# Kernel optimization log

Hardware: AMD Instinct MI355X
Metric: run time of the kernel (lower is better)

## Reference

```python
import jax, jax.numpy as jnp
import numpy as np

LN_EPS = 1e-5


def setup_inputs() -> dict:
    key = jax.random.key(0)
    ks = jax.random.split(key, 10)
    B, T, S, C = 8, 1024, 2048, 1024
    sd = 1.0 / np.sqrt(C)
    return {
        "x": jax.random.normal(ks[0], (B, T, C), jnp.float32),
        "lfb_feats": jax.random.normal(ks[1], (B, S, C), jnp.float32),
        "theta_w": jax.random.normal(ks[2], (C, C), jnp.float32) * sd,
        "theta_b": jax.random.normal(ks[3], (C,), jnp.float32) * 0.01,
        "phi_w": jax.random.normal(ks[4], (C, C), jnp.float32) * sd,
        "phi_b": jax.random.normal(ks[5], (C,), jnp.float32) * 0.01,
        "gi_w": jax.random.normal(ks[6], (C, C), jnp.float32) * sd,
        "gi_b": jax.random.normal(ks[7], (C,), jnp.float32) * 0.01,
        "ln_g": jnp.ones((C,), jnp.float32),
        "ln_b": jnp.zeros((C,), jnp.float32),
        "fc_w": jax.random.normal(ks[8], (C, C), jnp.float32) * sd,
        "fc_b": jax.random.normal(ks[9], (C,), jnp.float32) * 0.01,
    }


def _layernorm(h, g, b):
    mu = jnp.mean(h, axis=-1, keepdims=True)
    var = jnp.var(h, axis=-1, keepdims=True)
    return (h - mu) * jax.lax.rsqrt(var + LN_EPS) * g + b


def reference(x, lfb_feats, theta_w, theta_b, phi_w, phi_b, gi_w, gi_b,
              ln_g, ln_b, fc_w, fc_b):
    # x: [B,T,C], lfb_feats: [B,S,C]. 1x1 Conv1d == per-token linear on channels.
    C = x.shape[-1]
    scale = jnp.sqrt(jnp.asarray(C, x.dtype))  # NOTE: 1/sqrt(1/C) = sqrt(C) (as in source)
    theta = jnp.einsum('btc,oc->bto', x, theta_w) + theta_b          # [B,T,C]
    phi = jnp.einsum('bsc,oc->bso', lfb_feats, phi_w) + phi_b        # [B,S,C]
    gi = jnp.einsum('bsc,oc->bso', lfb_feats, gi_w) + gi_b           # [B,S,C]
    attn = jax.nn.softmax(jnp.einsum('btc,bsc->bts', theta, phi) * scale, axis=-1)
    out = jnp.einsum('bts,bsc->btc', attn, gi)                       # [B,T,C]
    out = jax.nn.relu(_layernorm(out, ln_g, ln_b))
    out = jnp.einsum('btc,oc->bto', out, fc_w) + fc_b                # fc (dropout = identity at eval)
    return out + x                                                   # residual, [B,T,C]
```

## Files before the change

kernel.cpp:

```cpp
#include <hip/hip_runtime.h>


#define BM 128
#define BN 128
#define BK 64

typedef __attribute__((ext_vector_type(8))) short short8;
typedef __attribute__((ext_vector_type(4))) float f32x4;
typedef __attribute__((ext_vector_type(4))) unsigned short us4;

enum { MODE_SPLIT = 0, MODE_TRANS = 1, MODE_F32 = 2, MODE_FINAL = 3 };

__device__ __forceinline__ float b2f(unsigned short u) {
  union { unsigned int i; float f; } x;
  x.i = ((unsigned int)u) << 16;
  return x.f;
}
__device__ __forceinline__ unsigned short f2b(float f) {
  unsigned int u = __float_as_uint(f);
  unsigned int r = (u + 0x7FFFu + ((u >> 16) & 1u)) >> 16;
  return (unsigned short)r;
}

__device__ __forceinline__ void async_cp16(const unsigned short* g,
                                           unsigned short* l) {
  __builtin_amdgcn_global_load_lds(
      (const __attribute__((address_space(1))) void*)g,
      (__attribute__((address_space(3))) void*)l, 16, 0, 0);
}

__global__ __launch_bounds__(256) void split_xlfb(
    const float* __restrict__ lfb, const float* __restrict__ x,
    const float* __restrict__ g, unsigned short* __restrict__ ls,
    unsigned short* __restrict__ xs, float* __restrict__ v, int Ms) {
  const int id = blockIdx.x;
  const int t = threadIdx.x;
  const int c = t * 4;
  if (id < Ms) {
    __shared__ float red[4];
    f32x4 xv = *(const f32x4*)&lfb[(size_t)id * 1024 + c];
    f32x4 gg = *(const f32x4*)&g[c];
    us4 hi, lo;
    float s = 0.f;
#pragma unroll
    for (int i = 0; i < 4; ++i) {
      hi[i] = f2b(xv[i]);
      lo[i] = f2b(xv[i] - b2f(hi[i]));
      s += xv[i] * gg[i];
    }
    *(us4*)&ls[(size_t)id * 2048 + c] = hi;
    *(us4*)&ls[(size_t)id * 2048 + 1024 + c] = lo;
    for (int o = 32; o; o >>= 1) s += __shfl_xor(s, o, 64);
    if ((t & 63) == 0) red[t >> 6] = s;
    __syncthreads();
    if (t == 0) v[id] = red[0] + red[1] + red[2] + red[3];
  } else {
    const int r = id - Ms;
    f32x4 xv = *(const f32x4*)&x[(size_t)r * 1024 + c];
    us4 hi, lo;
#pragma unroll
    for (int i = 0; i < 4; ++i) {
      hi[i] = f2b(xv[i]);
      lo[i] = f2b(xv[i] - b2f(hi[i]));
    }
    *(us4*)&xs[(size_t)r * 2048 + c] = hi;
    *(us4*)&xs[(size_t)r * 2048 + 1024 + c] = lo;
  }
}

__global__ __launch_bounds__(256) void cvt2_bf16(const float* __restrict__ s0,
                                                 unsigned short* __restrict__ d0,
                                                 const float* __restrict__ s1,
                                                 unsigned short* __restrict__ d1) {
  int b = blockIdx.x;
  const float* src = (b < 1024) ? s0 : s1;
  unsigned short* dst = (b < 1024) ? d0 : d1;
  int g = (b & 1023) * 256 + threadIdx.x;
  f32x4 v = *(const f32x4*)&src[g * 4];
  us4 o;
#pragma unroll
  for (int i = 0; i < 4; ++i) o[i] = f2b(v[i]);
  *(us4*)&dst[(size_t)g * 4] = o;
}

__global__ __launch_bounds__(256) void transpose_split2(
    const float* __restrict__ W0, unsigned short* __restrict__ T0,
    const float* __restrict__ W1, unsigned short* __restrict__ T1) {
  __shared__ float tile[64][65];
  const int sel = blockIdx.y >> 4;
  const float* W = sel ? W1 : W0;
  unsigned short* T = sel ? T1 : T0;
  const int bo = (blockIdx.y & 15) * 64;
  const int bc = blockIdx.x * 64;
  const int t = threadIdx.x;
  const int tr = t >> 4;
  const int tc = (t & 15) * 4;
#pragma unroll
  for (int i = 0; i < 4; ++i) {
    f32x4 v = *(const f32x4*)&W[(size_t)(bo + tr + 16 * i) * 1024 + bc + tc];
#pragma unroll
    for (int j = 0; j < 4; ++j) tile[tr + 16 * i][tc + j] = v[j];
  }
  __syncthreads();
#pragma unroll
  for (int i = 0; i < 4; ++i) {
    const int c = bc + tr + 16 * i;
    us4 hi, lo;
#pragma unroll
    for (int j = 0; j < 4; ++j) {
      float v = tile[tc + j][tr + 16 * i];
      hi[j] = f2b(v);
      lo[j] = f2b(v - b2f(hi[j]));
    }
    *(us4*)&T[(size_t)c * 2048 + bo + tc] = hi;
    *(us4*)&T[(size_t)c * 2048 + 1024 + bo + tc] = lo;
  }
}

__global__ __launch_bounds__(256) void make_g(
    const unsigned short* __restrict__ tB, const float* __restrict__ bth,
    float* __restrict__ g) {
  const int d = blockIdx.x * 4 + (threadIdx.x >> 6);
  const int lane = threadIdx.x & 63;
  float s = 0.f;
#pragma unroll
  for (int i = 0; i < 4; ++i) {
    const int o0 = lane * 4 + i * 256;
    us4 h = *(const us4*)&tB[(size_t)d * 2048 + o0];
    us4 lo = *(const us4*)&tB[(size_t)d * 2048 + 1024 + o0];
    f32x4 bb = *(const f32x4*)&bth[o0];
#pragma unroll
    for (int j = 0; j < 4; ++j) s += (b2f(h[j]) + b2f(lo[j])) * bb[j];
  }
  for (int o = 32; o; o >>= 1) s += __shfl_xor(s, o, 64);
  if (lane == 0) g[d] = s;
}

__global__ __launch_bounds__(256) void reduce_g(const float* __restrict__ P,
                                                unsigned short* __restrict__ Gs) {
  const int d = blockIdx.x;
  const int c = threadIdx.x * 4;
  f32x4 s = *(const f32x4*)&P[(size_t)d * 1024 + c];
#pragma unroll
  for (int z = 1; z < 8; ++z) {
    f32x4 p = *(const f32x4*)&P[(size_t)z * 1048576 + (size_t)d * 1024 + c];
#pragma unroll
    for (int i = 0; i < 4; ++i) s[i] += p[i];
  }
  us4 hi, lo;
#pragma unroll
  for (int i = 0; i < 4; ++i) {
    hi[i] = f2b(s[i]);
    lo[i] = f2b(s[i] - b2f(hi[i]));
  }
  *(us4*)&Gs[(size_t)d * 2048 + c] = hi;
  *(us4*)&Gs[(size_t)d * 2048 + 1024 + c] = lo;
}

template <int MODE>
__global__ __launch_bounds__(256, 4) void gemm_bt(
    const unsigned short* __restrict__ A, const unsigned short* __restrict__ B,
    void* __restrict__ Cout, const float* __restrict__ bias,
    const float* __restrict__ resid, int M, int N, int K, int lda, int ldb,
    int ldc, long long sA, long long sB, long long sC, long long sBias,
    int awrap, int awoff, int bwrap, int bwoff, int NBk, int MBk, int mbx,
    int swz, int kzoff) {
  __shared__ __align__(16) unsigned short As[BM * BK];
  __shared__ __align__(16) unsigned short Bs[BN * BK];

  const int tid = threadIdx.x;
  const int l = tid & 63;
  const int w = tid >> 6;
  const int wm = w >> 1, wn = w & 1;
  const int ln = l & 15, lq = l >> 4;

  int bmi, bni, bzi;
  {
    const int id = blockIdx.x;
    if (swz == 1) {
      bzi = id & 7;
      const int r = id >> 3;
      bmi = r % mbx;
      bni = r / mbx;
    } else if (swz == 2) {
      bzi = 0;
      const int r = id >> 3;
      bmi = (id & 7) * mbx + r % mbx;
      bni = r / mbx;
    } else {
      bni = id % NBk;
      const int rem = id / NBk;
      bmi = rem % MBk;
      bzi = rem / MBk;
    }
  }
  const int bm = bmi * BM;
  const int bn = bni * BN;
  const unsigned short* Ab = A + (size_t)bzi * (size_t)sA;
  const unsigned short* Bb = B + (size_t)bzi * (size_t)sB;
  const float* bz = bias ? bias + (size_t)bzi * (size_t)sBias : nullptr;
  const int kbase = bzi * kzoff;

  const int arow = tid >> 3;
  const int acol = (((tid & 7) ^ ((tid >> 3) & 7)) * 8);
  const int ldsbase = (tid & 0xC0) * 8;

  f32x4 acc[4][4];
#pragma unroll
  for (int i = 0; i < 4; ++i)
#pragma unroll
    for (int j = 0; j < 4; ++j) acc[i][j] = (f32x4){0.f, 0.f, 0.f, 0.f};

  const int sw = ln & 7;

  for (int k0 = 0; k0 < K; k0 += BK) {
    const int kg = k0 + kbase;
    const int ka = (kg < awrap) ? kg : kg - awoff;
    const int kb = (kg < bwrap) ? kg : kg - bwoff;
#pragma unroll
    for (int it = 0; it < 4; ++it) {
      const int r = it * 32 + arow;
      async_cp16(Ab + (size_t)(bm + r) * lda + ka + acol,
                 &As[it * 2048 + ldsbase]);
    }
#pragma unroll
    for (int it = 0; it < 4; ++it) {
      const int r = it * 32 + arow;
      async_cp16(Bb + (size_t)(bn + r) * ldb + kb + acol,
                 &Bs[it * 2048 + ldsbase]);
    }
    __syncthreads();

#pragma unroll
    for (int ks = 0; ks < 2; ++ks) {
      short8 a[4], b[4];
      const int kof = ((ks * 4 + lq) ^ sw) * 8;
#pragma unroll
      for (int i = 0; i < 4; ++i)
        a[i] = *(const short8*)&As[(wm * 64 + i * 16 + ln) * BK + kof];
#pragma unroll
      for (int j = 0; j < 4; ++j)
        b[j] = *(const short8*)&Bs[(wn * 64 + j * 16 + ln) * BK + kof];
#pragma unroll
      for (int i = 0; i < 4; ++i)
#pragma unroll
        for (int j = 0; j < 4; ++j)
          acc[i][j] = __builtin_amdgcn_mfma_f32_16x16x32_bf16(a[i], b[j],
                                                              acc[i][j], 0, 0, 0);
    }
    __syncthreads();
  }

  float* Cf = (float*)Cout + (size_t)bzi * (size_t)sC;
  unsigned short* Cb = (unsigned short*)Cout + (size_t)bzi * (size_t)sC;

  if constexpr (MODE == MODE_TRANS) {
#pragma unroll
    for (int i = 0; i < 4; ++i) {
      const int gm0 = bm + wm * 64 + i * 16 + lq * 4;
      const int bt = gm0 >> 11;
      const int sr = gm0 & 2047;
#pragma unroll
      for (int j = 0; j < 4; ++j) {
        const int gn = bn + wn * 64 + j * 16 + ln;
        const float bv2 = (bz != nullptr) ? bz[gn] : 0.f;
        us4 o;
#pragma unroll
        for (int r = 0; r < 4; ++r) o[r] = f2b(acc[i][j][r] + bv2);
        *(us4*)&Cb[(size_t)bt * 2097152 + (size_t)gn * 2048 + sr] = o;
      }
    }
  } else {
#pragma unroll
    for (int j = 0; j < 4; ++j) {
      const int gn = bn + wn * 64 + j * 16 + ln;
      const float bv2 = (bz != nullptr) ? bz[gn] : 0.f;
#pragma unroll
      for (int i = 0; i < 4; ++i) {
        const int gm0 = bm + wm * 64 + i * 16 + lq * 4;
#pragma unroll
        for (int r = 0; r < 4; ++r) {
          const int gm = gm0 + r;
          const float v = acc[i][j][r] + bv2;
          if constexpr (MODE == MODE_SPLIT) {
            unsigned short hi = f2b(v);
            Cb[(size_t)gm * ldc + gn] = hi;
            Cb[(size_t)gm * ldc + gn + (ldc >> 1)] = f2b(v - b2f(hi));
          } else if constexpr (MODE == MODE_F32) {
            Cf[(size_t)gm * ldc + gn] = v;
          } else if constexpr (MODE == MODE_FINAL) {
            const size_t idx = (size_t)gm * ldc + gn;
            Cf[idx] = v + resid[idx];
          }
        }
      }
    }
  }
}

__device__ __forceinline__ void ld8f(const unsigned short* Lb, int roff, int ln,
                                     int lq, int sw, short8* a) {
#pragma unroll
  for (int mi = 0; mi < 4; ++mi)
#pragma unroll
    for (int ks = 0; ks < 2; ++ks)
      a[mi * 2 + ks] = *(const short8*)&Lb[(roff + mi * 16 + ln) * 64 +
                                           (((ks * 4 + lq) ^ sw) * 8)];
}
__device__ __forceinline__ void ld4f(const unsigned short* Lb, int roff, int ln,
                                     int lq, int sw, short8* b) {
#pragma unroll
  for (int ni = 0; ni < 2; ++ni)
#pragma unroll
    for (int ks = 0; ks < 2; ++ks)
      b[ni * 2 + ks] = *(const short8*)&Lb[(roff + ni * 16 + ln) * 64 +
                                           (((ks * 4 + lq) ^ sw) * 8)];
}
template <int MH, int NH>
__device__ __forceinline__ void mfmaQ(f32x4 (&acc)[8][4], const short8* a,
                                      const short8* b) {
  __builtin_amdgcn_s_setprio(1);
#pragma unroll
  for (int mi = 0; mi < 4; ++mi)
#pragma unroll
    for (int ni = 0; ni < 2; ++ni)
#pragma unroll
      for (int ks = 0; ks < 2; ++ks)
        acc[MH * 4 + mi][NH * 2 + ni] = __builtin_amdgcn_mfma_f32_16x16x32_bf16(
            a[mi * 2 + ks], b[ni * 2 + ks], acc[MH * 4 + mi][NH * 2 + ni], 0, 0,
            0);
  __builtin_amdgcn_s_setprio(0);
}

template <int MODE>
__global__ __launch_bounds__(512, 1) void gemm8(
    const unsigned short* __restrict__ A, const unsigned short* __restrict__ B,
    void* __restrict__ Cout, const float* __restrict__ bias, int M, int N,
    int K, int lda, int ldb, int ldc, long long sA, long long sB, long long sC,
    long long sBias, int awrap, int awoff, int bwrap, int bwoff, int NBk,
    int MBk, int mbx, int swz) {
  __shared__ __align__(16) unsigned short lds[2][4][8192];

  const int tid = threadIdx.x;
  const int l = tid & 63;
  const int w = tid >> 6;
  const int wm = w >> 2;
  const int wn = w & 3;
  const int ln = l & 15, lq = l >> 4;
  const int sw = ln & 7;

  int bmi, bni, bzi;
  {
    const int id = blockIdx.x;
    if (swz == 1) {
      bzi = id & 7;
      const int r = id >> 3;
      bmi = r % mbx;
      bni = r / mbx;
    } else if (swz == 2) {
      bzi = 0;
      const int r = id >> 3;
      bmi = (id & 7) * mbx + r % mbx;
      bni = r / mbx;
    } else {
      bni = id % NBk;
      const int rem = id / NBk;
      bmi = rem % MBk;
      bzi = rem / MBk;
    }
  }
  const int bm = bmi * 256;
  const int bn = bni * 256;
  const unsigned short* Ab = A + (size_t)bzi * (size_t)sA;
  const unsigned short* Bb = B + (size_t)bzi * (size_t)sB;
  const float* bz = bias ? bias + (size_t)bzi * (size_t)sBias : nullptr;

  const int srow = tid >> 3;
  const int schk = ((tid & 7) ^ ((tid >> 3) & 7)) * 8;
  const int sdst0 = (tid & 448) * 8;

  auto stageA = [&](int d, int half, int kk) {
#pragma unroll
    for (int j = 0; j < 2; ++j)
      async_cp16(Ab + (size_t)(bm + half * 128 + srow + j * 64) * lda + kk +
                     schk,
                 &lds[d][half][sdst0 + j * 4096]);
  };
  auto stageB = [&](int d, int half, int kk) {
#pragma unroll
    for (int j = 0; j < 2; ++j)
      async_cp16(Bb + (size_t)(bn + half * 128 + srow + j * 64) * ldb + kk +
                     schk,
                 &lds[d][2 + half][sdst0 + j * 4096]);
  };
  auto wrapA = [&](int kg) { return (kg < awrap) ? kg : kg - awoff; };
  auto wrapB = [&](int kg) { return (kg < bwrap) ? kg : kg - bwoff; };

  f32x4 acc[8][4];
#pragma unroll
  for (int i = 0; i < 8; ++i)
#pragma unroll
    for (int j = 0; j < 4; ++j) acc[i][j] = (f32x4){0.f, 0.f, 0.f, 0.f};

  const int nt = K >> 6;

  stageA(0, 0, wrapA(0));
  stageA(0, 1, wrapA(0));
  stageB(0, 0, wrapB(0));
  stageB(0, 1, wrapB(0));
  if (nt > 1) {
    stageB(1, 0, wrapB(64));
    stageB(1, 1, wrapB(64));
    asm volatile("s_waitcnt vmcnt(4)" : : : "memory");
  } else {
    asm volatile("s_waitcnt vmcnt(0)" : : : "memory");
  }
  __builtin_amdgcn_s_barrier();

  const unsigned short* LA;
  const unsigned short* LB;
  short8 a0[8], a1[8], b0[4], b1[4];
  const int broff = (wn & 1) * 64;
  const int bslot = 2 + (wn >> 1);

  for (int t = 0; t < nt; ++t) {
    const int d = t & 1;
    LA = &lds[d][wm][0];
    LB = &lds[d][bslot][0];
    ld8f(LA, 0, ln, lq, sw, a0);
    ld4f(LB, broff, ln, lq, sw, b0);
    if (t + 1 < nt) stageA(d ^ 1, 0, wrapA((t + 1) * 64));
    __builtin_amdgcn_s_barrier();
    asm volatile("s_waitcnt lgkmcnt(0)" : : : "memory");
    __builtin_amdgcn_sched_barrier(0);
    mfmaQ<0, 0>(acc, a0, b0);
    __builtin_amdgcn_s_barrier();
    ld4f(LB, broff + 32, ln, lq, sw, b1);
    if (t + 1 < nt) stageA(d ^ 1, 1, wrapA((t + 1) * 64));
    __builtin_amdgcn_s_barrier();
    asm volatile("s_waitcnt lgkmcnt(0)" : : : "memory");
    __builtin_amdgcn_sched_barrier(0);
    mfmaQ<0, 1>(acc, a0, b1);
    __builtin_amdgcn_s_barrier();
    ld8f(LA, 64, ln, lq, sw, a1);
    if (t + 2 < nt) stageB(d, 0, wrapB((t + 2) * 64));
    __builtin_amdgcn_s_barrier();
    asm volatile("s_waitcnt lgkmcnt(0)" : : : "memory");
    __builtin_amdgcn_sched_barrier(0);
    mfmaQ<1, 1>(acc, a1, b1);
    __builtin_amdgcn_s_barrier();
    if (t + 2 < nt) stageB(d, 1, wrapB((t + 2) * 64));
    __builtin_amdgcn_s_barrier();
    mfmaQ<1, 0>(acc, a1, b0);
    if (t + 2 < nt) {
      asm volatile("s_waitcnt vmcnt(4)" : : : "memory");
    } else {
      asm volatile("s_waitcnt vmcnt(0)" : : : "memory");
    }
    __builtin_amdgcn_s_barrier();
  }

  float* Cf = (float*)Cout + (size_t)bzi * (size_t)sC;
  unsigned short* Cb = (unsigned short*)Cout;

  if constexpr (MODE == MODE_TRANS) {
#pragma unroll
    for (int mi = 0; mi < 8; ++mi) {
      const int gm0 = bm + wm * 128 + mi * 16 + lq * 4;
      const int bt = gm0 >> 11;
      const int sr = gm0 & 2047;
#pragma unroll
      for (int ni = 0; ni < 4; ++ni) {
        const int gn = bn + wn * 64 + ni * 16 + ln;
        const float bv2 = (bz != nullptr) ? bz[gn] : 0.f;
        us4 o;
#pragma unroll
        for (int r = 0; r < 4; ++r) o[r] = f2b(acc[mi][ni][r] + bv2);
        *(us4*)&Cb[(size_t)bt * 2097152 + (size_t)gn * 2048 + sr] = o;
      }
    }
  } else {
#pragma unroll
    for (int ni = 0; ni < 4; ++ni) {
      const int gn = bn + wn * 64 + ni * 16 + ln;
      const float bv2 = (bz != nullptr) ? bz[gn] : 0.f;
#pragma unroll
      for (int mi = 0; mi < 8; ++mi) {
        const int gm0 = bm + wm * 128 + mi * 16 + lq * 4;
#pragma unroll
        for (int r = 0; r < 4; ++r)
          Cf[(size_t)(gm0 + r) * ldc + gn] = acc[mi][ni][r] + bv2;
      }
    }
  }
}

__global__ __launch_bounds__(256) void softmax_rows(
    const float* __restrict__ logit, unsigned short* __restrict__ attn) {
  const int row = blockIdx.x;
  const float* L = logit + (size_t)row * 2048;
  unsigned short* O = attn + (size_t)row * 2048;
  const int t = threadIdx.x;
  __shared__ float red[8];

  f32x4 v0 = *(const f32x4*)&L[t * 4];
  f32x4 v1 = *(const f32x4*)&L[t * 4 + 1024];
  float m = fmaxf(fmaxf(fmaxf(v0[0], v0[1]), fmaxf(v0[2], v0[3])),
                  fmaxf(fmaxf(v1[0], v1[1]), fmaxf(v1[2], v1[3])));
  for (int o = 32; o; o >>= 1) m = fmaxf(m, __shfl_xor(m, o, 64));
  if ((t & 63) == 0) red[t >> 6] = m;
  __syncthreads();
  m = fmaxf(fmaxf(red[0], red[1]), fmaxf(red[2], red[3]));

  float e[8];
  float s = 0.f;
#pragma unroll
  for (int i = 0; i < 4; ++i) { e[i] = __expf(32.f * (v0[i] - m)); s += e[i]; }
#pragma unroll
  for (int i = 0; i < 4; ++i) { e[4 + i] = __expf(32.f * (v1[i] - m)); s += e[4 + i]; }
  for (int o = 32; o; o >>= 1) s += __shfl_xor(s, o, 64);
  if ((t & 63) == 0) red[4 + (t >> 6)] = s;
  __syncthreads();
  s = red[4] + red[5] + red[6] + red[7];
  const float inv = 1.f / s;
  us4 o0, o1;
#pragma unroll
  for (int i = 0; i < 4; ++i) { o0[i] = f2b(e[i] * inv); o1[i] = f2b(e[4 + i] * inv); }
  *(us4*)&O[t * 4] = o0;
  *(us4*)&O[t * 4 + 1024] = o1;
}

__global__ __launch_bounds__(256) void ln_relu(
    const float* __restrict__ X, const float* __restrict__ g,
    const float* __restrict__ b, unsigned short* __restrict__ H) {
  const int row = blockIdx.x;
  const float* x = X + (size_t)row * 1024;
  unsigned short* h = H + (size_t)row * 1024;
  const int t = threadIdx.x;
  __shared__ float red[8];
  f32x4 v = *(const f32x4*)&x[t * 4];
  float s = v[0] + v[1] + v[2] + v[3];
  float q = v[0] * v[0] + v[1] * v[1] + v[2] * v[2] + v[3] * v[3];
  for (int o = 32; o; o >>= 1) {
    s += __shfl_xor(s, o, 64);
    q += __shfl_xor(q, o, 64);
  }
  if ((t & 63) == 0) { red[t >> 6] = s; red[4 + (t >> 6)] = q; }
  __syncthreads();
  s = red[0] + red[1] + red[2] + red[3];
  q = red[4] + red[5] + red[6] + red[7];
  const float mean = s * (1.f / 1024.f);
  const float var = q * (1.f / 1024.f) - mean * mean;
  const float rstd = rsqrtf(var + 1e-5f);
  us4 o;
#pragma unroll
  for (int i = 0; i < 4; ++i) {
    const int c = t * 4 + i;
    const float y = (v[i] - mean) * rstd * g[c] + b[c];
    o[i] = f2b(fmaxf(y, 0.f));
  }
  *(us4*)&h[t * 4] = o;
}

extern "C" void kernel_launch(void* const* d_in, const int* in_sizes, int n_in,
                              void* d_out, int out_size, void* d_ws,
                              size_t ws_size, hipStream_t stream) {
  const float* x = (const float*)d_in[0];
  const float* lfb = (const float*)d_in[1];
  const float* th_w = (const float*)d_in[2];
  const float* th_b = (const float*)d_in[3];
  const float* ph_w = (const float*)d_in[4];
  const float* gi_w = (const float*)d_in[6];
  const float* gi_b = (const float*)d_in[7];
  const float* lng = (const float*)d_in[8];
  const float* lnb = (const float*)d_in[9];
  const float* fc_w = (const float*)d_in[10];
  const float* fc_b = (const float*)d_in[11];
  float* outf = (float*)d_out;
  char* ws = (char*)d_ws;

  const size_t MB = 1048576;
  int nb = 1;
  for (int cand = 8; cand >= 1; cand >>= 1)
    if ((size_t)cand * 24 * MB + 18 * MB <= ws_size) { nb = cand; break; }

  char* tail = ws + (size_t)nb * 24 * MB;
  unsigned short* tA = (unsigned short*)(tail);
  unsigned short* tB = (unsigned short*)(tail + 4 * MB);
  unsigned short* Gs = (unsigned short*)(tail + 8 * MB);
  unsigned short* giw = (unsigned short*)(tail + 12 * MB);
  unsigned short* fcw = (unsigned short*)(tail + 14 * MB);
  float* gv = (float*)(tail + 16 * MB);
  float* vb = (float*)(tail + 16 * MB + 65536);

  dim3 blk(256);
  transpose_split2<<<dim3(16, 32), blk, 0, stream>>>(th_w, tA, ph_w, tB);
  make_g<<<dim3(256), blk, 0, stream>>>(tB, th_b, gv);
  if (nb >= 2) {
    float* gpart = (float*)ws;
    gemm_bt<MODE_F32><<<dim3(512), blk, 0, stream>>>(
        tB, tA, gpart, nullptr, nullptr, 1024, 1024, 384, 2048, 2048, 1024,
        0, 0, 1048576LL, 0, 2048, 2048, 1024, 1024, 8, 8, 8, 1, 384);
    reduce_g<<<dim3(1024), blk, 0, stream>>>(gpart, Gs);
  } else {
    gemm_bt<MODE_SPLIT><<<dim3(64), blk, 0, stream>>>(
        tB, tA, Gs, nullptr, nullptr, 1024, 1024, 3072, 2048, 2048, 2048,
        0, 0, 0, 0, 2048, 2048, 1024, 1024, 8, 8, 1, 2, 0);
  }
  cvt2_bf16<<<dim3(2048), blk, 0, stream>>>(gi_w, giw, fc_w, fcw);

  for (int b0 = 0; b0 < 8; b0 += nb) {
    unsigned short* xs = (unsigned short*)(ws);
    float* logit = (float*)(ws);
    unsigned short* ls = (unsigned short*)(ws + (size_t)nb * 8 * MB);
    unsigned short* ys = (unsigned short*)(ws + (size_t)nb * 16 * MB);
    unsigned short* giT = (unsigned short*)(ws + (size_t)nb * 20 * MB);
    unsigned short* attn = ys;
    float* outp = (float*)ws;
    unsigned short* h = giT;

    const float* xb = x + (size_t)b0 * 1048576;
    const float* lfbb = lfb + (size_t)b0 * 2097152;
    float* ob = outf + (size_t)b0 * 1048576;
    const int Ms = nb * 2048;
    const int Mt = nb * 1024;
    const int zswz = (nb == 8) ? 1 : 0;

    split_xlfb<<<dim3(Ms + Mt), blk, 0, stream>>>(lfbb, xb, gv, ls, xs, vb, Ms);
    gemm8<MODE_TRANS><<<dim3(32 * nb), dim3(512), 0, stream>>>(
        ls, giw, giT, gi_b, Ms, 1024, 1024, 2048, 1024, 2048,
        0LL, 0LL, 0LL, 0LL, 1024, 0, 1024, 0, 4, 8 * nb, nb, 2);
    gemm_bt<MODE_SPLIT><<<dim3(8 * (Mt / 128)), blk, 0, stream>>>(
        xs, Gs, ys, nullptr, nullptr, Mt, 1024, 3072, 2048, 2048, 2048,
        0, 0, 0, 0, 2048, 2048, 1024, 1024, 8, Mt / 128, Mt / 1024, 2, 0);
    gemm8<MODE_F32><<<dim3(32 * nb), dim3(512), 0, stream>>>(
        ys, ls, logit, vb, 1024, 2048, 3072, 2048, 2048, 2048,
        2097152LL, 4194304LL, 2097152LL, 2048LL, 2048, 2048, 1024, 1024,
        8, 4, 4, zswz);
    softmax_rows<<<dim3(Mt), blk, 0, stream>>>(logit, attn);
    gemm_bt<MODE_F32><<<dim3(8 * 8 * nb), blk, 0, stream>>>(
        attn, giT, outp, nullptr, nullptr, 1024, 1024, 2048, 2048, 2048, 1024,
        2097152LL, 2097152LL, 1048576LL, 0, 2048, 0, 2048, 0, 8, 8, 8, zswz, 0);
    ln_relu<<<dim3(Mt), blk, 0, stream>>>(outp, lng, lnb, h);
    gemm_bt<MODE_FINAL><<<dim3(8 * (Mt / 128)), blk, 0, stream>>>(
        h, fcw, ob, fc_b, xb, Mt, 1024, 1024, 1024, 1024, 1024,
        0, 0, 0, 0, 1024, 0, 1024, 0, 8, Mt / 128, Mt / 1024, 2, 0);
  }
}
```

Baseline: 501.3 us.

## Collapse GEMM main loop to two barriers by issuing all LDS fragment loads upfront

```diff
diff --git a/kernel.cpp b/kernel.cpp
--- a/kernel.cpp
+++ b/kernel.cpp
@@ -339,7 +339,8 @@
     int K, int lda, int ldb, int ldc, long long sA, long long sB, long long sC,
     long long sBias, int awrap, int awoff, int bwrap, int bwoff, int NBk,
     int MBk, int mbx, int swz) {
-  __shared__ __align__(16) unsigned short lds[2][4][8192];
+  __shared__ __align__(16) unsigned short Abuf[2][2][8192];
+  __shared__ __align__(16) unsigned short Bbuf[2][2][8192];
 
   const int tid = threadIdx.x;
   const int l = tid & 63;
@@ -379,19 +380,23 @@
   const int schk = ((tid & 7) ^ ((tid >> 3) & 7)) * 8;
   const int sdst0 = (tid & 448) * 8;
 
-  auto stageA = [&](int d, int half, int kk) {
-#pragma unroll
-    for (int j = 0; j < 2; ++j)
-      async_cp16(Ab + (size_t)(bm + half * 128 + srow + j * 64) * lda + kk +
-                     schk,
-                 &lds[d][half][sdst0 + j * 4096]);
+  auto stageA = [&](int d, int kk) {
+#pragma unroll
+    for (int half = 0; half < 2; ++half)
+#pragma unroll
+      for (int j = 0; j < 2; ++j)
+        async_cp16(Ab + (size_t)(bm + half * 128 + srow + j * 64) * lda + kk +
+                       schk,
+                   &Abuf[d][half][sdst0 + j * 4096]);
   };
-  auto stageB = [&](int d, int half, int kk) {
-#pragma unroll
-    for (int j = 0; j < 2; ++j)
-      async_cp16(Bb + (size_t)(bn + half * 128 + srow + j * 64) * ldb + kk +
-                     schk,
-                 &lds[d][2 + half][sdst0 + j * 4096]);
+  auto stageB = [&](int d, int kk) {
+#pragma unroll
+    for (int half = 0; half < 2; ++half)
+#pragma unroll
+      for (int j = 0; j < 2; ++j)
+        async_cp16(Bb + (size_t)(bn + half * 128 + srow + j * 64) * ldb + kk +
+                       schk,
+                   &Bbuf[d][half][sdst0 + j * 4096]);
   };
   auto wrapA = [&](int kg) { return (kg < awrap) ? kg : kg - awoff; };
   auto wrapB = [&](int kg) { return (kg < bwrap) ? kg : kg - bwoff; };
@@ -404,59 +409,42 @@
 
   const int nt = K >> 6;
 
-  stageA(0, 0, wrapA(0));
-  stageA(0, 1, wrapA(0));
-  stageB(0, 0, wrapB(0));
-  stageB(0, 1, wrapB(0));
+  stageA(0, wrapA(0));
+  stageB(0, wrapB(0));
   if (nt > 1) {
-    stageB(1, 0, wrapB(64));
-    stageB(1, 1, wrapB(64));
+    stageB(1, wrapB(64));
     asm volatile("s_waitcnt vmcnt(4)" : : : "memory");
   } else {
     asm volatile("s_waitcnt vmcnt(0)" : : : "memory");
   }
+  __builtin_amdgcn_sched_barrier(0);
   __builtin_amdgcn_s_barrier();
 
-  const unsigned short* LA;
-  const unsigned short* LB;
   short8 a0[8], a1[8], b0[4], b1[4];
   const int broff = (wn & 1) * 64;
-  const int bslot = 2 + (wn >> 1);
+  const int bhalf = wn >> 1;
 
   for (int t = 0; t < nt; ++t) {
-    const int d = t & 1;
-    LA = &lds[d][wm][0];
-    LB = &lds[d][bslot][0];
+    const int p = t & 1;
+    const unsigned short* LA = &Abuf[p][wm][0];
+    const unsigned short* LB = &Bbuf[p][bhalf][0];
     ld8f(LA, 0, ln, lq, sw, a0);
     ld4f(LB, broff, ln, lq, sw, b0);
-    if (t + 1 < nt) stageA(d ^ 1, 0, wrapA((t + 1) * 64));
-    __builtin_amdgcn_s_barrier();
-    asm volatile("s_waitcnt lgkmcnt(0)" : : : "memory");
-    __builtin_amdgcn_sched_barrier(0);
+    ld4f(LB, broff + 32, ln, lq, sw, b1);
+    ld8f(LA, 64, ln, lq, sw, a1);
+    if (t + 1 < nt) stageA(p ^ 1, wrapA((t + 1) * 64));
     mfmaQ<0, 0>(acc, a0, b0);
-    __builtin_amdgcn_s_barrier();
-    ld4f(LB, broff + 32, ln, lq, sw, b1);
-    if (t + 1 < nt) stageA(d ^ 1, 1, wrapA((t + 1) * 64));
-    __builtin_amdgcn_s_barrier();
-    asm volatile("s_waitcnt lgkmcnt(0)" : : : "memory");
-    __builtin_amdgcn_sched_barrier(0);
     mfmaQ<0, 1>(acc, a0, b1);
     __builtin_amdgcn_s_barrier();
-    ld8f(LA, 64, ln, lq, sw, a1);
-    if (t + 2 < nt) stageB(d, 0, wrapB((t + 2) * 64));
-    __builtin_amdgcn_s_barrier();
-    asm volatile("s_waitcnt lgkmcnt(0)" : : : "memory");
-    __builtin_amdgcn_sched_barrier(0);
+    if (t + 2 < nt) stageB(p, wrapB((t + 2) * 64));
     mfmaQ<1, 1>(acc, a1, b1);
-    __builtin_amdgcn_s_barrier();
-    if (t + 2 < nt) stageB(d, 1, wrapB((t + 2) * 64));
-    __builtin_amdgcn_s_barrier();
     mfmaQ<1, 0>(acc, a1, b0);
     if (t + 2 < nt) {
       asm volatile("s_waitcnt vmcnt(4)" : : : "memory");
     } else {
       asm volatile("s_waitcnt vmcnt(0)" : : : "memory");
     }
+    __builtin_amdgcn_sched_barrier(0);
     __builtin_amdgcn_s_barrier();
   }
 
```

New measurement: 502.7 us. About the same (+0.3%).
